# Performance work log

Hardware: AMD Instinct MI355X
Metric: run time of the kernel (lower is better)

Reference implementation:

```python
import jax, jax.numpy as jnp
import numpy as np

D_MODEL = 1024
D_STATE = 64
D_CONV = 4
EXPAND = 2
HEADDIM = 64
FFN_MULT = 3
MEM_DIM = 256
D_INNER = EXPAND * D_MODEL            # 2048
NHEADS = D_INNER // HEADDIM           # 32
CONV_DIM = D_INNER + 2 * D_STATE      # x, B, C channels through the causal conv
D_IN_PROJ = 2 * D_INNER + 2 * D_STATE + NHEADS  # z, xBC, dt
FFN_HID = FFN_MULT * D_MODEL


def _rms(x, eps=1e-6):
    return x * jax.lax.rsqrt(jnp.mean(x * x, axis=-1, keepdims=True) + eps)


def _mamba2(u, in_proj_w, conv_w, conv_b, dt_bias, A_log, D_param, mnorm_w, out_proj_w):
    # u: [B, L, d_model]
    Bsz, L, _ = u.shape
    zxbcdt = u @ in_proj_w.T                                  # [B, L, D_IN_PROJ]
    z = zxbcdt[..., :D_INNER]                                 # gate branch
    xBC = zxbcdt[..., D_INNER:D_INNER + CONV_DIM]
    dt = zxbcdt[..., D_INNER + CONV_DIM:]                     # [B, L, H]
    # causal depthwise conv1d (kernel D_CONV) + silu
    xp = jnp.pad(xBC, ((0, 0), (D_CONV - 1, 0), (0, 0)))
    xBC = sum(xp[:, k:k + L, :] * conv_w[:, k] for k in range(D_CONV)) + conv_b
    xBC = jax.nn.silu(xBC)
    xh = xBC[..., :D_INNER].reshape(Bsz, L, NHEADS, HEADDIM)  # [B, L, H, P]
    Bm = xBC[..., D_INNER:D_INNER + D_STATE]                  # [B, L, N] (ngroups=1)
    Cm = xBC[..., D_INNER + D_STATE:]                         # [B, L, N]
    dt = jax.nn.softplus(dt + dt_bias)                        # [B, L, H]
    dA = jnp.exp(dt * (-jnp.exp(A_log)))                      # [B, L, H]

    def step(h, inp):
        # h: [B, H, P, N]
        da, dtt, xt, bt, ct = inp
        h = da[:, :, None, None] * h + jnp.einsum('bh,bhp,bn->bhpn', dtt, xt, bt)
        y = jnp.einsum('bhpn,bn->bhp', h, ct)
        return h, y

    h0 = jnp.zeros((Bsz, NHEADS, HEADDIM, D_STATE), u.dtype)
    xs = (jnp.moveaxis(dA, 1, 0), jnp.moveaxis(dt, 1, 0), jnp.moveaxis(xh, 1, 0),
          jnp.moveaxis(Bm, 1, 0), jnp.moveaxis(Cm, 1, 0))
    _, ys = jax.lax.scan(step, h0, xs)                        # ys: [L, B, H, P]
    y = jnp.moveaxis(ys, 0, 1) + D_param[None, None, :, None] * xh
    y = y.reshape(Bsz, L, D_INNER)
    y = _rms(y * jax.nn.silu(z)) * mnorm_w                    # RMSNormGated
    return y @ out_proj_w.T


def setup_inputs() -> dict:
    key = jax.random.key(0)
    ks = jax.random.split(key, 12)
    B, L = 1, 2048
    s = 0.02
    return {
        'x': jax.random.normal(ks[0], (B, L, D_MODEL), jnp.float32),
        'x0': jax.random.normal(ks[1], (B, L, D_MODEL), jnp.float32),
        'mem': jax.random.normal(ks[2], (B, MEM_DIM), jnp.float32),
        'resid_mix': jnp.stack([jnp.ones(D_MODEL), jnp.zeros(D_MODEL)]),
        'ssm_scale': jnp.ones(D_MODEL),
        'mlp_scale': jnp.ones(D_MODEL),
        'ssm_norm_w': jnp.ones(D_MODEL),
        'ffn_norm_w': jnp.ones(D_MODEL),
        'in_proj_w': jax.random.normal(ks[3], (D_IN_PROJ, D_MODEL), jnp.float32) * s,
        'conv_w': jax.random.normal(ks[4], (CONV_DIM, D_CONV), jnp.float32) * 0.2,
        'conv_b': jnp.zeros(CONV_DIM),
        'dt_bias': jax.random.uniform(ks[5], (NHEADS,), jnp.float32, -2.0, 0.0),
        'A_log': jnp.log(jnp.linspace(1.0, 16.0, NHEADS).astype(jnp.float32)),
        'D_param': jnp.ones(NHEADS),
        'mnorm_w': jnp.ones(D_INNER),
        'out_proj_w': jax.random.normal(ks[6], (D_MODEL, D_INNER), jnp.float32) * s,
        'gate_up_w': jax.random.normal(ks[7], (2 * FFN_HID, D_MODEL), jnp.float32) * s,
        'down_w': jax.random.normal(ks[8], (D_MODEL, FFN_HID), jnp.float32) * s,
    }


def reference(x, x0, mem, resid_mix, ssm_scale, mlp_scale, ssm_norm_w, ffn_norm_w,
              in_proj_w, conv_w, conv_b, dt_bias, A_log, D_param, mnorm_w,
              out_proj_w, gate_up_w, down_w):
    # residual mixing (USE_MEMORY=0, so mem path is inert)
    x = resid_mix[0][None, None, :] * x + resid_mix[1][None, None, :] * x0
    y = _mamba2(_rms(x) * ssm_norm_w, in_proj_w, conv_w, conv_b, dt_bias,
                A_log, D_param, mnorm_w, out_proj_w)
    x = x + ssm_scale[None, None, :] * y
    # SwiGLU FFN
    h = _rms(x) * ffn_norm_w
    gu = h @ gate_up_w.T
    gate, up = jnp.split(gu, 2, axis=-1)
    x = x + mlp_scale[None, None, :] * ((jax.nn.silu(gate) * up) @ down_w.T)
    return x
```

## Files before the change

kernel.cpp:

```cpp
#include <hip/hip_runtime.h>
#include <hip/hip_bf16.h>
#include <math.h>

#define LSEQ 2048
#define DMODEL 1024
#define DINNER 2048
#define NHEADS 32
#define HEADDIM 64
#define DSTATE 64
#define CONVDIM 2176
#define XBCDT_W 2304
#define FFNHID 3072

typedef float f32x4 __attribute__((ext_vector_type(4)));
typedef __bf16 bf16x8 __attribute__((ext_vector_type(8)));
typedef __hip_bfloat16 bf16;

__device__ __forceinline__ float siluf(float x){ return x / (1.0f + expf(-x)); }

#define GLOAD_LDS16(gp, lp) __builtin_amdgcn_global_load_lds( \
    (const __attribute__((address_space(1))) void*)(gp), \
    (__attribute__((address_space(3))) void*)(lp), 16, 0, 0)

__device__ __forceinline__ float block_reduce_sum_256(float v){
  #pragma unroll
  for (int o = 32; o > 0; o >>= 1) v += __shfl_down(v, o, 64);
  __shared__ float sh[4];
  int lane = threadIdx.x & 63;
  int w = threadIdx.x >> 6;
  if (lane == 0) sh[w] = v;
  __syncthreads();
  return sh[0] + sh[1] + sh[2] + sh[3];
}

__device__ __forceinline__ ushort bf16bits(float f){
  __hip_bfloat16 h = __float2bfloat16(f);
  return *reinterpret_cast<ushort*>(&h);
}

__device__ __forceinline__ int swz64(int r, int c){
  return r*64 + ((((c>>3) ^ (r&7)))<<3) + (c&7);
}

__global__ __launch_bounds__(256) void k_castmix(
    const float* __restrict__ w0, const float* __restrict__ w1,
    const float* __restrict__ w2, const float* __restrict__ w3,
    bf16* __restrict__ d0, bf16* __restrict__ d1,
    bf16* __restrict__ d2, bf16* __restrict__ d3,
    const float* __restrict__ x, const float* __restrict__ x0,
    const float* __restrict__ rm, const float* __restrict__ nw,
    float* __restrict__ xres, bf16* __restrict__ u)
{
  int tid = threadIdx.x;
  if (blockIdx.x < 15616){
    int idx = blockIdx.x * 256 + tid;
    const float* s; bf16* d; int valid;
    if (idx < 1114112)      { s = w0; d = d0; valid = 1089536; }
    else if (idx < 1638400) { idx -= 1114112; s = w1; d = d1; valid = 524288; }
    else if (idx < 3211264) { idx -= 1638400; s = w2; d = d2; valid = 1572864; }
    else                    { idx -= 3211264; s = w3; d = d3; valid = 786432; }
    float4 v = (idx < valid) ? *(const float4*)(s + (size_t)idx * 4)
                             : make_float4(0.f, 0.f, 0.f, 0.f);
    ushort4 r;
    r.x = bf16bits(v.x); r.y = bf16bits(v.y); r.z = bf16bits(v.z); r.w = bf16bits(v.w);
    *(ushort4*)(d + (size_t)idx * 4) = r;
    return;
  }
  int row = blockIdx.x - 15616;
  float4 xv  = ((const float4*)(x  + (size_t)row * DMODEL))[tid];
  float4 x0v = ((const float4*)(x0 + (size_t)row * DMODEL))[tid];
  float4 r0 = ((const float4*)rm)[tid];
  float4 r1 = ((const float4*)(rm + DMODEL))[tid];
  float4 a;
  a.x = r0.x*xv.x + r1.x*x0v.x; a.y = r0.y*xv.y + r1.y*x0v.y;
  a.z = r0.z*xv.z + r1.z*x0v.z; a.w = r0.w*xv.w + r1.w*x0v.w;
  ((float4*)(xres + (size_t)row * DMODEL))[tid] = a;
  float ss = a.x*a.x + a.y*a.y + a.z*a.z + a.w*a.w;
  ss = block_reduce_sum_256(ss);
  float inv = rsqrtf(ss / (float)DMODEL + 1e-6f);
  float4 nv = ((const float4*)nw)[tid];
  ushort4 o;
  o.x = bf16bits(a.x*inv*nv.x); o.y = bf16bits(a.y*inv*nv.y);
  o.z = bf16bits(a.z*inv*nv.z); o.w = bf16bits(a.w*inv*nv.w);
  *(ushort4*)(u + (size_t)row * DMODEL + tid*4) = o;
}

__device__ __forceinline__ void xcdswz2(int &bx, int &by){
  int gx = gridDim.x;
  int nblk = gx * gridDim.y;
  int flat = by * gx + bx;
  flat = (flat & 7) * (nblk >> 3) + (flat >> 3);
  by = flat / gx; bx = flat - by * gx;
}

__device__ __forceinline__ void gemm_mainloop128(
    const bf16* __restrict__ A, const bf16* __restrict__ W,
    int ld, int Klen, bf16* As, bf16* Ws, f32x4 acc[4][4])
{
  int tid = threadIdx.x, lane = tid & 63, wid = tid >> 6;
  int wm = (wid >> 1) * 64, wn = (wid & 1) * 64;
  int r16 = lane & 15, g8 = lane >> 4;
  int srow = lane >> 2;
  int scol = ((lane & 3) ^ (srow & 3)) * 8;
  const bf16* ga0 = A + (size_t)(wid*32 + srow) * ld + scol;
  const bf16* ga1 = ga0 + (size_t)16 * ld;
  const bf16* gw0 = W + (size_t)(wid*32 + srow) * ld + scol;
  const bf16* gw1 = gw0 + (size_t)16 * ld;
  GLOAD_LDS16(ga0, As + wid*1024);
  GLOAD_LDS16(ga1, As + wid*1024 + 512);
  GLOAD_LDS16(gw0, Ws + wid*1024);
  GLOAD_LDS16(gw1, Ws + wid*1024 + 512);
  __syncthreads();
  int cur = 0, s4 = (r16 & 3) * 8;
  for (int k0 = 0; k0 < Klen; k0 += 32){
    if (k0 + 32 < Klen){
      int nb = (cur ^ 1) * 4096;
      GLOAD_LDS16(ga0 + k0 + 32, As + nb + wid*1024);
      GLOAD_LDS16(ga1 + k0 + 32, As + nb + wid*1024 + 512);
      GLOAD_LDS16(gw0 + k0 + 32, Ws + nb + wid*1024);
      GLOAD_LDS16(gw1 + k0 + 32, Ws + nb + wid*1024 + 512);
    }
    int cb = cur * 4096;
    bf16x8 af[4], bfr[4];
    #pragma unroll
    for (int i = 0; i < 4; ++i)
      af[i] = *(const bf16x8*)(As + cb + (wm + i*16 + r16)*32 + (g8*8 ^ s4));
    #pragma unroll
    for (int j = 0; j < 4; ++j)
      bfr[j] = *(const bf16x8*)(Ws + cb + (wn + j*16 + r16)*32 + (g8*8 ^ s4));
    #pragma unroll
    for (int i = 0; i < 4; ++i)
      #pragma unroll
      for (int j = 0; j < 4; ++j)
        acc[i][j] = __builtin_amdgcn_mfma_f32_16x16x32_bf16(af[i], bfr[j], acc[i][j], 0, 0, 0);
    __syncthreads();
    cur ^= 1;
  }
}

__global__ __launch_bounds__(256) void k_gemm_inproj(
    const bf16* __restrict__ A, const bf16* __restrict__ Wfull,
    float* __restrict__ zbuf, float* __restrict__ xbcdt)
{
  __shared__ __align__(16) bf16 As[2*4096];
  __shared__ __align__(16) bf16 Ws[2*4096];
  int bx = blockIdx.x, by = blockIdx.y;
  xcdswz2(bx, by);
  f32x4 acc[4][4];
  #pragma unroll
  for (int i = 0; i < 4; ++i)
    #pragma unroll
    for (int j = 0; j < 4; ++j) acc[i][j] = (f32x4){0.f,0.f,0.f,0.f};
  gemm_mainloop128(A + (size_t)(by*128)*DMODEL, Wfull + (size_t)(bx*128)*DMODEL,
                   DMODEL, DMODEL, As, Ws, acc);
  int tid = threadIdx.x, lane = tid & 63, wid = tid >> 6;
  int wm = (wid >> 1) * 64, wn = (wid & 1) * 64;
  int r16 = lane & 15, g8 = lane >> 4;
  float* Cp; int ldc, col0;
  if (bx < 16){ Cp = zbuf;  ldc = DINNER;  col0 = bx*128; }
  else        { Cp = xbcdt; ldc = XBCDT_W; col0 = (bx-16)*128; }
  #pragma unroll
  for (int i = 0; i < 4; ++i){
    int row = by*128 + wm + i*16 + g8*4;
    #pragma unroll
    for (int j = 0; j < 4; ++j){
      int col = col0 + wn + j*16 + r16;
      #pragma unroll
      for (int r = 0; r < 4; ++r)
        Cp[(size_t)(row + r) * ldc + col] = acc[i][j][r];
    }
  }
}

__global__ __launch_bounds__(256) void k_gemm_splitk(
    const bf16* __restrict__ A, const bf16* __restrict__ W,
    float* __restrict__ P, int Kfull, int Kq, int N)
{
  __shared__ __align__(16) bf16 As[2*4096];
  __shared__ __align__(16) bf16 Ws[2*4096];
  int gx = gridDim.x, gxy = gx * gridDim.y;
  int nblk = gxy * gridDim.z;
  int flat = blockIdx.z * gxy + blockIdx.y * gx + blockIdx.x;
  flat = (flat & 7) * (nblk >> 3) + (flat >> 3);
  int z = flat / gxy; int rem = flat - z * gxy;
  int by = rem / gx, bx = rem - by * gx;
  f32x4 acc[4][4];
  #pragma unroll
  for (int i = 0; i < 4; ++i)
    #pragma unroll
    for (int j = 0; j < 4; ++j) acc[i][j] = (f32x4){0.f,0.f,0.f,0.f};
  gemm_mainloop128(A + (size_t)(by*128)*Kfull + z*Kq,
                   W + (size_t)(bx*128)*Kfull + z*Kq,
                   Kfull, Kq, As, Ws, acc);
  float* Pz = P + (size_t)z * LSEQ * N;
  int tid = threadIdx.x, lane = tid & 63, wid = tid >> 6;
  int wm = (wid >> 1) * 64, wn = (wid & 1) * 64;
  int r16 = lane & 15, g8 = lane >> 4;
  #pragma unroll
  for (int i = 0; i < 4; ++i){
    int row = by*128 + wm + i*16 + g8*4;
    #pragma unroll
    for (int j = 0; j < 4; ++j){
      int col = bx*128 + wn + j*16 + r16;
      #pragma unroll
      for (int r = 0; r < 4; ++r)
        Pz[(size_t)(row + r) * N + col] = acc[i][j][r];
    }
  }
}

__global__ __launch_bounds__(256) void k_gemm_ffn(
    const bf16* __restrict__ A, const bf16* __restrict__ Wg, const bf16* __restrict__ Wu,
    bf16* __restrict__ act, int K)
{
  __shared__ __align__(16) bf16 As[2*4096];
  __shared__ __align__(16) bf16 Ws[2*4096];
  int bx = blockIdx.x, by = blockIdx.y;
  xcdswz2(bx, by);
  int tid = threadIdx.x, lane = tid & 63, wid = tid >> 6;
  int wm = (wid >> 1) * 64, wc = (wid & 1) * 32;
  int r16 = lane & 15, g8 = lane >> 4;
  int srow = lane >> 2;
  int scol = ((lane & 3) ^ (srow & 3)) * 8;
  const bf16* ga0 = A + (size_t)(by*128 + wid*32 + srow) * K + scol;
  const bf16* ga1 = ga0 + (size_t)16 * K;
  const bf16* gwsrc = (wid < 2) ? Wg : Wu;
  const bf16* gw0 = gwsrc + (size_t)(bx*64 + (wid & 1)*32 + srow) * K + scol;
  const bf16* gw1 = gw0 + (size_t)16 * K;
  f32x4 accg[4][2], accu[4][2];
  #pragma unroll
  for (int i = 0; i < 4; ++i)
    #pragma unroll
    for (int j = 0; j < 2; ++j){
      accg[i][j] = (f32x4){0.f,0.f,0.f,0.f};
      accu[i][j] = (f32x4){0.f,0.f,0.f,0.f};
    }
  GLOAD_LDS16(ga0, As + wid*1024);
  GLOAD_LDS16(ga1, As + wid*1024 + 512);
  GLOAD_LDS16(gw0, Ws + wid*1024);
  GLOAD_LDS16(gw1, Ws + wid*1024 + 512);
  __syncthreads();
  int cur = 0, s4 = (r16 & 3) * 8;
  for (int k0 = 0; k0 < K; k0 += 32){
    if (k0 + 32 < K){
      int nb = (cur ^ 1) * 4096;
      GLOAD_LDS16(ga0 + k0 + 32, As + nb + wid*1024);
      GLOAD_LDS16(ga1 + k0 + 32, As + nb + wid*1024 + 512);
      GLOAD_LDS16(gw0 + k0 + 32, Ws + nb + wid*1024);
      GLOAD_LDS16(gw1 + k0 + 32, Ws + nb + wid*1024 + 512);
    }
    int cb = cur * 4096;
    bf16x8 af[4], gf[2], uf[2];
    #pragma unroll
    for (int i = 0; i < 4; ++i)
      af[i] = *(const bf16x8*)(As + cb + (wm + i*16 + r16)*32 + (g8*8 ^ s4));
    #pragma unroll
    for (int j = 0; j < 2; ++j){
      int gr = wc + j*16 + r16;
      int ur = 64 + wc + j*16 + r16;
      gf[j] = *(const bf16x8*)(Ws + cb + gr*32 + (g8*8 ^ s4));
      uf[j] = *(const bf16x8*)(Ws + cb + ur*32 + (g8*8 ^ s4));
    }
    #pragma unroll
    for (int i = 0; i < 4; ++i)
      #pragma unroll
      for (int j = 0; j < 2; ++j){
        accg[i][j] = __builtin_amdgcn_mfma_f32_16x16x32_bf16(af[i], gf[j], accg[i][j], 0, 0, 0);
        accu[i][j] = __builtin_amdgcn_mfma_f32_16x16x32_bf16(af[i], uf[j], accu[i][j], 0, 0, 0);
      }
    __syncthreads();
    cur ^= 1;
  }
  #pragma unroll
  for (int i = 0; i < 4; ++i){
    int row = by*128 + wm + i*16 + g8*4;
    #pragma unroll
    for (int j = 0; j < 2; ++j){
      int col = bx*64 + wc + j*16 + r16;
      #pragma unroll
      for (int r = 0; r < 4; ++r){
        float g = accg[i][j][r], u = accu[i][j][r];
        act[(size_t)(row + r) * FFNHID + col] = __float2bfloat16(siluf(g) * u);
      }
    }
  }
}

__global__ __launch_bounds__(256) void k_convdt(
    const float* __restrict__ xbcdt, const float* __restrict__ cw,
    const float* __restrict__ cb, const float* __restrict__ dtb,
    const float* __restrict__ alog, float* __restrict__ xbc,
    float* __restrict__ dtv, float* __restrict__ lav)
{
  int idx = blockIdx.x * 256 + threadIdx.x;
  if (idx >= LSEQ * 2208) return;
  int l = idx / 2208, c = idx - l * 2208;
  if (c < CONVDIM){
    float acc = cb[c];
    #pragma unroll
    for (int k = 0; k < 4; ++k){
      int t = l + k - 3;
      if (t >= 0) acc = fmaf(xbcdt[(size_t)t * XBCDT_W + c], cw[c*4 + k], acc);
    }
    xbc[(size_t)l * CONVDIM + c] = siluf(acc);
  } else {
    int h = c - CONVDIM;
    float raw = xbcdt[(size_t)l * XBCDT_W + c] + dtb[h];
    float d = (raw > 20.f) ? raw : log1pf(expf(raw));
    dtv[l * NHEADS + h] = d;
    lav[l * NHEADS + h] = -expf(alog[h]) * d;
  }
}

__global__ __launch_bounds__(256) void k_scanA(
    const float* __restrict__ xbc, const float* __restrict__ dtv,
    const float* __restrict__ lav, float* __restrict__ T, float* __restrict__ ctot)
{
  __shared__ bf16 sXw[4096];
  __shared__ bf16 sBt[4096];
  __shared__ float scum[64], swt[64];
  int h = blockIdx.x >> 5, c = blockIdx.x & 31;
  int tid = threadIdx.x, t0 = c * 64;
  if (tid < 64){
    float cum = lav[(size_t)(t0 + tid) * NHEADS + h];
    #pragma unroll
    for (int o = 1; o < 64; o <<= 1){
      float v = __shfl_up(cum, o, 64);
      if (tid >= o) cum += v;
    }
    scum[tid] = cum;
  }
  __syncthreads();
  float Lc = scum[63];
  if (tid < 64)
    swt[tid] = expf(Lc - scum[tid]) * dtv[(size_t)(t0 + tid) * NHEADS + h];
  __syncthreads();
  for (int idx = tid; idx < 4096; idx += 256){
    int j = idx >> 6, n = idx & 63;
    size_t rb = (size_t)(t0 + j) * CONVDIM;
    sXw[swz64(n, j)] = __float2bfloat16(xbc[rb + h * HEADDIM + n] * swt[j]);
    sBt[swz64(n, j)] = __float2bfloat16(xbc[rb + DINNER + n]);
  }
  __syncthreads();
  int lane = tid & 63, wid = tid >> 6;
  int wr = (wid >> 1) * 32, wc = (wid & 1) * 32;
  int r16 = lane & 15, g8 = lane >> 4;
  f32x4 acc[2][2];
  #pragma unroll
  for (int i = 0; i < 2; ++i)
    #pragma unroll
    for (int j = 0; j < 2; ++j) acc[i][j] = (f32x4){0.f,0.f,0.f,0.f};
  #pragma unroll
  for (int kk = 0; kk < 2; ++kk){
    int ks = kk*4 + g8;
    bf16x8 a[2], b[2];
    #pragma unroll
    for (int i = 0; i < 2; ++i){
      int row = wr + i*16 + r16;
      a[i] = *(const bf16x8*)(sXw + row*64 + ((ks ^ (row&7))<<3));
    }
    #pragma unroll
    for (int j = 0; j < 2; ++j){
      int row = wc + j*16 + r16;
      b[j] = *(const bf16x8*)(sBt + row*64 + ((ks ^ (row&7))<<3));
    }
    #pragma unroll
    for (int i = 0; i < 2; ++i)
      #pragma unroll
      for (int j = 0; j < 2; ++j)
        acc[i][j] = __builtin_amdgcn_mfma_f32_16x16x32_bf16(a[i], b[j], acc[i][j], 0, 0, 0);
  }
  float* Tb = T + (size_t)blockIdx.x * 4096;
  #pragma unroll
  for (int i = 0; i < 2; ++i)
    #pragma unroll
    for (int j = 0; j < 2; ++j)
      #pragma unroll
      for (int r = 0; r < 4; ++r){
        int p = wr + i*16 + g8*4 + r, n = wc + j*16 + r16;
        Tb[p*64 + n] = acc[i][j][r];
      }
  if (tid == 0) ctot[blockIdx.x] = expf(Lc);
}

__global__ __launch_bounds__(256) void k_scanB(float* __restrict__ T, const float* __restrict__ ctot)
{
  int h = blockIdx.x >> 3, e = blockIdx.x & 7;
  int tid = threadIdx.x;
  size_t off = (size_t)e * 512 + tid * 2;
  float s0 = 0.f, s1 = 0.f;
  for (int c = 0; c < 32; ++c){
    float ct = ctot[h * 32 + c];
    size_t base = (size_t)(h * 32 + c) * 4096 + off;
    float2 tv = *(const float2*)&T[base];
    *(float2*)&T[base] = make_float2(s0, s1);
    s0 = fmaf(ct, s0, tv.x);
    s1 = fmaf(ct, s1, tv.y);
  }
}

__global__ __launch_bounds__(256) void k_scanC(
    const float* __restrict__ xbc, const float* __restrict__ Sin,
    const float* __restrict__ dtv, const float* __restrict__ lav,
    const float* __restrict__ Dp, float* __restrict__ y)
{
  __shared__ bf16 sC[4096];
  __shared__ bf16 sBS[4096];
  __shared__ bf16 sXt[4096];
  __shared__ bf16 sXr[4096];
  __shared__ bf16 sSb[4096];
  __shared__ float scum[64], sdt[64];
  int h = blockIdx.x >> 5, c = blockIdx.x & 31;
  int tid = threadIdx.x, t0 = c * 64;
  if (tid < 64){
    float cum = lav[(size_t)(t0 + tid) * NHEADS + h];
    #pragma unroll
    for (int o = 1; o < 64; o <<= 1){
      float v = __shfl_up(cum, o, 64);
      if (tid >= o) cum += v;
    }
    scum[tid] = cum;
    sdt[tid] = dtv[(size_t)(t0 + tid) * NHEADS + h];
  }
  for (int idx = tid; idx < 4096; idx += 256){
    int j = idx >> 6, n = idx & 63;
    size_t rb = (size_t)(t0 + j) * CONVDIM;
    float xv = xbc[rb + h * HEADDIM + n];
    sC [swz64(j, n)] = __float2bfloat16(xbc[rb + DINNER + DSTATE + n]);
    sBS[swz64(j, n)] = __float2bfloat16(xbc[rb + DINNER + n]);
    sXr[swz64(j, n)] = __float2bfloat16(xv);
    sXt[swz64(n, j)] = __float2bfloat16(xv);
    sSb[swz64(j, n)] = __float2bfloat16(Sin[(size_t)blockIdx.x * 4096 + idx]);
  }
  __syncthreads();
  int lane = tid & 63, wid = tid >> 6;
  int wr = (wid >> 1) * 32, wc = (wid & 1) * 32;
  int r16 = lane & 15, g8 = lane >> 4;
  f32x4 gacc[2][2];
  #pragma unroll
  for (int i = 0; i < 2; ++i)
    #pragma unroll
    for (int j = 0; j < 2; ++j) gacc[i][j] = (f32x4){0.f,0.f,0.f,0.f};
  #pragma unroll
  for (int kk = 0; kk < 2; ++kk){
    int ks = kk*4 + g8;
    bf16x8 a[2], b[2];
    #pragma unroll
    for (int i = 0; i < 2; ++i){
      int row = wr + i*16 + r16;
      a[i] = *(const bf16x8*)(sC + row*64 + ((ks ^ (row&7))<<3));
    }
    #pragma unroll
    for (int j = 0; j < 2; ++j){
      int row = wc + j*16 + r16;
      b[j] = *(const bf16x8*)(sBS + row*64 + ((ks ^ (row&7))<<3));
    }
    #pragma unroll
    for (int i = 0; i < 2; ++i)
      #pragma unroll
      for (int j = 0; j < 2; ++j)
        gacc[i][j] = __builtin_amdgcn_mfma_f32_16x16x32_bf16(a[i], b[j], gacc[i][j], 0, 0, 0);
  }
  __syncthreads();
  #pragma unroll
  for (int i = 0; i < 2; ++i)
    #pragma unroll
    for (int j = 0; j < 2; ++j)
      #pragma unroll
      for (int r = 0; r < 4; ++r){
        int i_ = wr + i*16 + g8*4 + r, j_ = wc + j*16 + r16;
        float v = (j_ <= i_) ? gacc[i][j][r] * expf(scum[i_] - scum[j_]) * sdt[j_] : 0.f;
        sBS[swz64(i_, j_)] = __float2bfloat16(v);
      }
  __syncthreads();
  f32x4 a1[2][2], a2[2][2];
  #pragma unroll
  for (int i = 0; i < 2; ++i)
    #pragma unroll
    for (int j = 0; j < 2; ++j){
      a1[i][j] = (f32x4){0.f,0.f,0.f,0.f};
      a2[i][j] = (f32x4){0.f,0.f,0.f,0.f};
    }
  #pragma unroll
  for (int kk = 0; kk < 2; ++kk){
    int ks = kk*4 + g8;
    bf16x8 sa[2], xa[2], ca[2], sb[2];
    #pragma unroll
    for (int i = 0; i < 2; ++i){
      int row = wr + i*16 + r16;
      sa[i] = *(const bf16x8*)(sBS + row*64 + ((ks ^ (row&7))<<3));
      ca[i] = *(const bf16x8*)(sC  + row*64 + ((ks ^ (row&7))<<3));
    }
    #pragma unroll
    for (int j = 0; j < 2; ++j){
      int row = wc + j*16 + r16;
      xa[j] = *(const bf16x8*)(sXt + row*64 + ((ks ^ (row&7))<<3));
      sb[j] = *(const bf16x8*)(sSb + row*64 + ((ks ^ (row&7))<<3));
    }
    #pragma unroll
    for (int i = 0; i < 2; ++i)
      #pragma unroll
      for (int j = 0; j < 2; ++j){
        a1[i][j] = __builtin_amdgcn_mfma_f32_16x16x32_bf16(sa[i], xa[j], a1[i][j], 0, 0, 0);
        a2[i][j] = __builtin_amdgcn_mfma_f32_16x16x32_bf16(ca[i], sb[j], a2[i][j], 0, 0, 0);
      }
  }
  float Dh = Dp[h];
  #pragma unroll
  for (int i = 0; i < 2; ++i)
    #pragma unroll
    for (int r = 0; r < 4; ++r){
      int i_ = wr + i*16 + g8*4 + r;
      float wi = expf(scum[i_]);
      #pragma unroll
      for (int j = 0; j < 2; ++j){
        int p_ = wc + j*16 + r16;
        float xv = __bfloat162float(sXr[swz64(i_, p_)]);
        y[(size_t)(t0 + i_) * DINNER + h * HEADDIM + p_] =
            a1[i][j][r] + wi * a2[i][j][r] + Dh * xv;
      }
    }
}

__global__ __launch_bounds__(256) void k_gate_rms(
    const float* __restrict__ y, const float* __restrict__ zbuf,
    const float* __restrict__ mw, bf16* __restrict__ yn)
{
  int row = blockIdx.x, tid = threadIdx.x;
  const float4* yr = (const float4*)(y    + (size_t)row * DINNER);
  const float4* zr = (const float4*)(zbuf + (size_t)row * DINNER);
  float4 v[2]; float ss = 0.f;
  #pragma unroll
  for (int i = 0; i < 2; ++i){
    int d4 = tid + i * 256;
    float4 yv = yr[d4], zv = zr[d4];
    float4 g;
    g.x = yv.x * siluf(zv.x); g.y = yv.y * siluf(zv.y);
    g.z = yv.z * siluf(zv.z); g.w = yv.w * siluf(zv.w);
    v[i] = g;
    ss += g.x*g.x + g.y*g.y + g.z*g.z + g.w*g.w;
  }
  ss = block_reduce_sum_256(ss);
  float inv = rsqrtf(ss / (float)DINNER + 1e-6f);
  #pragma unroll
  for (int i = 0; i < 2; ++i){
    int d4 = tid + i * 256;
    float4 mv = ((const float4*)mw)[d4];
    ushort4 o;
    o.x = bf16bits(v[i].x*inv*mv.x); o.y = bf16bits(v[i].y*inv*mv.y);
    o.z = bf16bits(v[i].z*inv*mv.z); o.w = bf16bits(v[i].w*inv*mv.w);
    *(ushort4*)(yn + (size_t)row * DINNER + d4*4) = o;
  }
}

__global__ __launch_bounds__(256) void k_res_rms(
    const float* __restrict__ xres, const float* __restrict__ yoP,
    const float* __restrict__ scale, const float* __restrict__ nw,
    float* __restrict__ x2, bf16* __restrict__ hb)
{
  int row = blockIdx.x, tid = threadIdx.x;
  const size_t PS = (size_t)LSEQ * DMODEL;
  float4 xv = ((const float4*)(xres + (size_t)row * DMODEL))[tid];
  float4 y0 = ((const float4*)(yoP          + (size_t)row * DMODEL))[tid];
  float4 y1 = ((const float4*)(yoP +   PS   + (size_t)row * DMODEL))[tid];
  float4 y2 = ((const float4*)(yoP + 2*PS   + (size_t)row * DMODEL))[tid];
  float4 y3 = ((const float4*)(yoP + 3*PS   + (size_t)row * DMODEL))[tid];
  float4 sv = ((const float4*)scale)[tid];
  float4 a;
  a.x = xv.x + sv.x*(y0.x+y1.x+y2.x+y3.x);
  a.y = xv.y + sv.y*(y0.y+y1.y+y2.y+y3.y);
  a.z = xv.z + sv.z*(y0.z+y1.z+y2.z+y3.z);
  a.w = xv.w + sv.w*(y0.w+y1.w+y2.w+y3.w);
  ((float4*)(x2 + (size_t)row * DMODEL))[tid] = a;
  float ss = a.x*a.x + a.y*a.y + a.z*a.z + a.w*a.w;
  ss = block_reduce_sum_256(ss);
  float inv = rsqrtf(ss / (float)DMODEL + 1e-6f);
  float4 nv = ((const float4*)nw)[tid];
  ushort4 o;
  o.x = bf16bits(a.x*inv*nv.x); o.y = bf16bits(a.y*inv*nv.y);
  o.z = bf16bits(a.z*inv*nv.z); o.w = bf16bits(a.w*inv*nv.w);
  *(ushort4*)(hb + (size_t)row * DMODEL + tid*4) = o;
}

__global__ __launch_bounds__(256) void k_final(
    const float* __restrict__ x2, const float* __restrict__ dP,
    const float* __restrict__ mscale, float* __restrict__ out)
{
  int i4 = blockIdx.x * 256 + threadIdx.x;
  const size_t PS4 = (size_t)LSEQ * DMODEL / 4;
  float4 xv = ((const float4*)x2)[i4];
  float4 a  = ((const float4*)dP)[i4];
  float4 b  = ((const float4*)dP)[i4 + PS4];
  float4 c  = ((const float4*)dP)[i4 + 2*PS4];
  float4 d  = ((const float4*)dP)[i4 + 3*PS4];
  float4 mv = ((const float4*)mscale)[i4 & 255];
  float4 o;
  o.x = xv.x + mv.x*(a.x+b.x+c.x+d.x);
  o.y = xv.y + mv.y*(a.y+b.y+c.y+d.y);
  o.z = xv.z + mv.z*(a.z+b.z+c.z+d.z);
  o.w = xv.w + mv.w*(a.w+b.w+c.w+d.w);
  ((float4*)out)[i4] = o;
}

extern "C" void kernel_launch(void* const* d_in, const int* in_sizes, int n_in,
                              void* d_out, int out_size, void* d_ws, size_t ws_size,
                              hipStream_t stream)
{
  const float* x      = (const float*)d_in[0];
  const float* x0     = (const float*)d_in[1];
  const float* rm     = (const float*)d_in[3];
  const float* sscale = (const float*)d_in[4];
  const float* mscale = (const float*)d_in[5];
  const float* snw    = (const float*)d_in[6];
  const float* fnw    = (const float*)d_in[7];
  const float* win    = (const float*)d_in[8];
  const float* cw     = (const float*)d_in[9];
  const float* cb     = (const float*)d_in[10];
  const float* dtb    = (const float*)d_in[11];
  const float* alog   = (const float*)d_in[12];
  const float* Dp     = (const float*)d_in[13];
  const float* mnw    = (const float*)d_in[14];
  const float* wout   = (const float*)d_in[15];
  const float* wgu    = (const float*)d_in[16];
  const float* wdn    = (const float*)d_in[17];
  float* out = (float*)d_out;

  const size_t MB = 1024ull * 1024ull;
  char* ws = (char*)d_ws;
  bf16*  woutb = (bf16*) (ws + 0*MB);
  bf16*  wgub  = (bf16*) (ws + 4*MB);
  bf16*  wdnb  = (bf16*) (ws + 16*MB);
  float* xres  = (float*)(ws + 22*MB);
  bf16*  winb  = (bf16*) (ws + 30*MB);
  bf16*  u     = (bf16*) (ws + 39*MB);
  float* dtv   = (float*)(ws + 39*MB);
  float* lav   = (float*)(ws + 39*MB + 256*1024);
  bf16*  hb    = (bf16*) (ws + 39*MB);
  float* zbuf  = (float*)(ws + 43*MB);
  float* x2    = (float*)(ws + 43*MB);
  float* xbcdt = (float*)(ws + 59*MB);
  float* yb    = (float*)(ws + 59*MB);
  float* yoP   = (float*)(ws + 59*MB);
  bf16*  act   = (bf16*) (ws + 59*MB);
  float* dP    = (float*)(ws + 71*MB);
  float* xbc   = (float*)(ws + 77*MB);
  float* T     = (float*)(ws + 95*MB);
  bf16*  yn    = (bf16*) (ws + 95*MB);
  float* ctot  = (float*)(ws + 112*MB);

  dim3 blk(256);
  k_castmix<<<17664, blk, 0, stream>>>(win, wout, wgu, wdn, winb, woutb, wgub, wdnb,
                                       x, x0, rm, snw, xres, u);
  k_gemm_inproj<<<dim3(34,16), blk, 0, stream>>>(u, winb, zbuf, xbcdt);
  k_convdt<<<(LSEQ*2208 + 255)/256, blk, 0, stream>>>(xbcdt, cw, cb, dtb, alog, xbc, dtv, lav);
  k_scanA<<<NHEADS*32, blk, 0, stream>>>(xbc, dtv, lav, T, ctot);
  k_scanB<<<NHEADS*8, blk, 0, stream>>>(T, ctot);
  k_scanC<<<NHEADS*32, blk, 0, stream>>>(xbc, T, dtv, lav, Dp, yb);
  k_gate_rms<<<LSEQ, blk, 0, stream>>>(yb, zbuf, mnw, yn);
  k_gemm_splitk<<<dim3(8,16,4), blk, 0, stream>>>(yn, woutb, yoP, DINNER, DINNER/4, DMODEL);
  k_res_rms<<<LSEQ, blk, 0, stream>>>(xres, yoP, sscale, fnw, x2, hb);
  k_gemm_ffn<<<dim3(48,16), blk, 0, stream>>>(hb, wgub, wgub + (size_t)FFNHID*DMODEL, act, DMODEL);
  k_gemm_splitk<<<dim3(8,16,4), blk, 0, stream>>>(act, wdnb, dP, FFNHID, FFNHID/4, DMODEL);
  k_final<<<2048, blk, 0, stream>>>(x2, dP, mscale, out);
}
```

Measured before the change: 211.7 us.

## Store SSM intermediates in bf16 and vectorize conv/scan loads

```diff
diff --git a/kernel.cpp b/kernel.cpp
--- a/kernel.cpp
+++ b/kernel.cpp
@@ -36,6 +36,9 @@
 __device__ __forceinline__ ushort bf16bits(float f){
   __hip_bfloat16 h = __float2bfloat16(f);
   return *reinterpret_cast<ushort*>(&h);
+}
+__device__ __forceinline__ float bfu(ushort u){
+  union { float f; unsigned int i; } w; w.i = ((unsigned int)u) << 16; return w.f;
 }
 
 __device__ __forceinline__ int swz64(int r, int c){
@@ -140,7 +143,7 @@
 
 __global__ __launch_bounds__(256) void k_gemm_inproj(
     const bf16* __restrict__ A, const bf16* __restrict__ Wfull,
-    float* __restrict__ zbuf, float* __restrict__ xbcdt)
+    bf16* __restrict__ zbuf, bf16* __restrict__ xbcdt)
 {
   __shared__ __align__(16) bf16 As[2*4096];
   __shared__ __align__(16) bf16 Ws[2*4096];
@@ -156,7 +159,7 @@
   int tid = threadIdx.x, lane = tid & 63, wid = tid >> 6;
   int wm = (wid >> 1) * 64, wn = (wid & 1) * 64;
   int r16 = lane & 15, g8 = lane >> 4;
-  float* Cp; int ldc, col0;
+  bf16* Cp; int ldc, col0;
   if (bx < 16){ Cp = zbuf;  ldc = DINNER;  col0 = bx*128; }
   else        { Cp = xbcdt; ldc = XBCDT_W; col0 = (bx-16)*128; }
   #pragma unroll
@@ -167,7 +170,7 @@
       int col = col0 + wn + j*16 + r16;
       #pragma unroll
       for (int r = 0; r < 4; ++r)
-        Cp[(size_t)(row + r) * ldc + col] = acc[i][j][r];
+        Cp[(size_t)(row + r) * ldc + col] = __float2bfloat16(acc[i][j][r]);
     }
   }
 }
@@ -287,37 +290,60 @@
 }
 
 __global__ __launch_bounds__(256) void k_convdt(
-    const float* __restrict__ xbcdt, const float* __restrict__ cw,
+    const bf16* __restrict__ xbcdt, const float* __restrict__ cw,
     const float* __restrict__ cb, const float* __restrict__ dtb,
-    const float* __restrict__ alog, float* __restrict__ xbc,
+    const float* __restrict__ alog, bf16* __restrict__ xbc,
     float* __restrict__ dtv, float* __restrict__ lav)
 {
   int idx = blockIdx.x * 256 + threadIdx.x;
-  if (idx >= LSEQ * 2208) return;
-  int l = idx / 2208, c = idx - l * 2208;
-  if (c < CONVDIM){
-    float acc = cb[c];
+  int l = idx / 552, q = idx - l * 552;
+  if (l >= LSEQ) return;
+  if (q < 544){
+    int c = q * 4;
+    float4 bv = *(const float4*)(cb + c);
+    float acc0 = bv.x, acc1 = bv.y, acc2 = bv.z, acc3 = bv.w;
+    float4 w0 = *(const float4*)(cw + (size_t)(c+0)*4);
+    float4 w1 = *(const float4*)(cw + (size_t)(c+1)*4);
+    float4 w2 = *(const float4*)(cw + (size_t)(c+2)*4);
+    float4 w3 = *(const float4*)(cw + (size_t)(c+3)*4);
+    const float* w0p = (const float*)&w0;
+    const float* w1p = (const float*)&w1;
+    const float* w2p = (const float*)&w2;
+    const float* w3p = (const float*)&w3;
     #pragma unroll
     for (int k = 0; k < 4; ++k){
       int t = l + k - 3;
-      if (t >= 0) acc = fmaf(xbcdt[(size_t)t * XBCDT_W + c], cw[c*4 + k], acc);
-    }
-    xbc[(size_t)l * CONVDIM + c] = siluf(acc);
+      if (t < 0) continue;
+      ushort4 rv = *(const ushort4*)(xbcdt + (size_t)t * XBCDT_W + c);
+      acc0 = fmaf(bfu(rv.x), w0p[k], acc0);
+      acc1 = fmaf(bfu(rv.y), w1p[k], acc1);
+      acc2 = fmaf(bfu(rv.z), w2p[k], acc2);
+      acc3 = fmaf(bfu(rv.w), w3p[k], acc3);
+    }
+    ushort4 o;
+    o.x = bf16bits(siluf(acc0)); o.y = bf16bits(siluf(acc1));
+    o.z = bf16bits(siluf(acc2)); o.w = bf16bits(siluf(acc3));
+    *(ushort4*)(xbc + (size_t)l * CONVDIM + c) = o;
   } else {
-    int h = c - CONVDIM;
-    float raw = xbcdt[(size_t)l * XBCDT_W + c] + dtb[h];
-    float d = (raw > 20.f) ? raw : log1pf(expf(raw));
-    dtv[l * NHEADS + h] = d;
-    lav[l * NHEADS + h] = -expf(alog[h]) * d;
+    int h0 = (q - 544) * 4;
+    ushort4 rv = *(const ushort4*)(xbcdt + (size_t)l * XBCDT_W + CONVDIM + h0);
+    float raws[4] = { bfu(rv.x), bfu(rv.y), bfu(rv.z), bfu(rv.w) };
+    #pragma unroll
+    for (int i = 0; i < 4; ++i){
+      float raw = raws[i] + dtb[h0 + i];
+      float d = (raw > 20.f) ? raw : log1pf(expf(raw));
+      dtv[l * NHEADS + h0 + i] = d;
+      lav[l * NHEADS + h0 + i] = -expf(alog[h0 + i]) * d;
+    }
   }
 }
 
 __global__ __launch_bounds__(256) void k_scanA(
-    const float* __restrict__ xbc, const float* __restrict__ dtv,
+    const bf16* __restrict__ xbc, const float* __restrict__ dtv,
     const float* __restrict__ lav, float* __restrict__ T, float* __restrict__ ctot)
 {
-  __shared__ bf16 sXw[4096];
-  __shared__ bf16 sBt[4096];
+  __shared__ __bf16 sXw[4096];
+  __shared__ __bf16 sBt[4096];
   __shared__ float scum[64], swt[64];
   int h = blockIdx.x >> 5, c = blockIdx.x & 31;
   int tid = threadIdx.x, t0 = c * 64;
@@ -335,11 +361,17 @@
   if (tid < 64)
     swt[tid] = expf(Lc - scum[tid]) * dtv[(size_t)(t0 + tid) * NHEADS + h];
   __syncthreads();
-  for (int idx = tid; idx < 4096; idx += 256){
-    int j = idx >> 6, n = idx & 63;
-    size_t rb = (size_t)(t0 + j) * CONVDIM;
-    sXw[swz64(n, j)] = __float2bfloat16(xbc[rb + h * HEADDIM + n] * swt[j]);
-    sBt[swz64(n, j)] = __float2bfloat16(xbc[rb + DINNER + n]);
+  for (int idx = tid; idx < 512; idx += 256){
+    int j = idx >> 3, n0 = (idx & 7) * 8;
+    const bf16* rb = xbc + (size_t)(t0 + j) * CONVDIM;
+    bf16x8 x8 = *(const bf16x8*)(rb + h * HEADDIM + n0);
+    bf16x8 b8 = *(const bf16x8*)(rb + DINNER + n0);
+    float wj = swt[j];
+    #pragma unroll
+    for (int e = 0; e < 8; ++e){
+      sXw[swz64(n0 + e, j)] = (__bf16)((float)x8[e] * wj);
+      sBt[swz64(n0 + e, j)] = b8[e];
+    }
   }
   __syncthreads();
   int lane = tid & 63, wid = tid >> 6;
@@ -400,15 +432,15 @@
 }
 
 __global__ __launch_bounds__(256) void k_scanC(
-    const float* __restrict__ xbc, const float* __restrict__ Sin,
+    const bf16* __restrict__ xbc, const float* __restrict__ Sin,
     const float* __restrict__ dtv, const float* __restrict__ lav,
-    const float* __restrict__ Dp, float* __restrict__ y)
-{
-  __shared__ bf16 sC[4096];
-  __shared__ bf16 sBS[4096];
-  __shared__ bf16 sXt[4096];
-  __shared__ bf16 sXr[4096];
-  __shared__ bf16 sSb[4096];
+    const float* __restrict__ Dp, bf16* __restrict__ y)
+{
+  __shared__ __bf16 sC[4096];
+  __shared__ __bf16 sBS[4096];
+  __shared__ __bf16 sXt[4096];
+  __shared__ __bf16 sXr[4096];
+  __shared__ __bf16 sSb[4096];
   __shared__ float scum[64], sdt[64];
   int h = blockIdx.x >> 5, c = blockIdx.x & 31;
   int tid = threadIdx.x, t0 = c * 64;
@@ -422,15 +454,25 @@
     scum[tid] = cum;
     sdt[tid] = dtv[(size_t)(t0 + tid) * NHEADS + h];
   }
-  for (int idx = tid; idx < 4096; idx += 256){
-    int j = idx >> 6, n = idx & 63;
-    size_t rb = (size_t)(t0 + j) * CONVDIM;
-    float xv = xbc[rb + h * HEADDIM + n];
-    sC [swz64(j, n)] = __float2bfloat16(xbc[rb + DINNER + DSTATE + n]);
-    sBS[swz64(j, n)] = __float2bfloat16(xbc[rb + DINNER + n]);
-    sXr[swz64(j, n)] = __float2bfloat16(xv);
-    sXt[swz64(n, j)] = __float2bfloat16(xv);
-    sSb[swz64(j, n)] = __float2bfloat16(Sin[(size_t)blockIdx.x * 4096 + idx]);
+  for (int idx = tid; idx < 512; idx += 256){
+    int j = idx >> 3, n0 = (idx & 7) * 8;
+    const bf16* rb = xbc + (size_t)(t0 + j) * CONVDIM;
+    bf16x8 x8 = *(const bf16x8*)(rb + h * HEADDIM + n0);
+    bf16x8 c8 = *(const bf16x8*)(rb + DINNER + DSTATE + n0);
+    bf16x8 b8 = *(const bf16x8*)(rb + DINNER + n0);
+    *(bf16x8*)(sC  + swz64(j, n0)) = c8;
+    *(bf16x8*)(sBS + swz64(j, n0)) = b8;
+    *(bf16x8*)(sXr + swz64(j, n0)) = x8;
+    const float* sp = Sin + (size_t)blockIdx.x * 4096 + j*64 + n0;
+    float4 s0 = *(const float4*)sp;
+    float4 s1 = *(const float4*)(sp + 4);
+    bf16x8 sv;
+    sv[0] = (__bf16)s0.x; sv[1] = (__bf16)s0.y; sv[2] = (__bf16)s0.z; sv[3] = (__bf16)s0.w;
+    sv[4] = (__bf16)s1.x; sv[5] = (__bf16)s1.y; sv[6] = (__bf16)s1.z; sv[7] = (__bf16)s1.w;
+    *(bf16x8*)(sSb + swz64(j, n0)) = sv;
+    #pragma unroll
+    for (int e = 0; e < 8; ++e)
+      sXt[swz64(n0 + e, j)] = x8[e];
   }
   __syncthreads();
   int lane = tid & 63, wid = tid >> 6;
@@ -470,7 +512,7 @@
       for (int r = 0; r < 4; ++r){
         int i_ = wr + i*16 + g8*4 + r, j_ = wc + j*16 + r16;
         float v = (j_ <= i_) ? gacc[i][j][r] * expf(scum[i_] - scum[j_]) * sdt[j_] : 0.f;
-        sBS[swz64(i_, j_)] = __float2bfloat16(v);
+        sBS[swz64(i_, j_)] = (__bf16)v;
       }
   __syncthreads();
   f32x4 a1[2][2], a2[2][2];
@@ -515,42 +557,38 @@
       #pragma unroll
       for (int j = 0; j < 2; ++j){
         int p_ = wc + j*16 + r16;
-        float xv = __bfloat162float(sXr[swz64(i_, p_)]);
+        float xv = (float)sXr[swz64(i_, p_)];
         y[(size_t)(t0 + i_) * DINNER + h * HEADDIM + p_] =
-            a1[i][j][r] + wi * a2[i][j][r] + Dh * xv;
+            __float2bfloat16(a1[i][j][r] + wi * a2[i][j][r] + Dh * xv);
       }
     }
 }
 
 __global__ __launch_bounds__(256) void k_gate_rms(
-    const float* __restrict__ y, const float* __restrict__ zbuf,
+    const bf16* __restrict__ y, const bf16* __restrict__ zbuf,
     const float* __restrict__ mw, bf16* __restrict__ yn)
 {
   int row = blockIdx.x, tid = threadIdx.x;
-  const float4* yr = (const float4*)(y    + (size_t)row * DINNER);
-  const float4* zr = (const float4*)(zbuf + (size_t)row * DINNER);
-  float4 v[2]; float ss = 0.f;
-  #pragma unroll
-  for (int i = 0; i < 2; ++i){
-    int d4 = tid + i * 256;
-    float4 yv = yr[d4], zv = zr[d4];
-    float4 g;
-    g.x = yv.x * siluf(zv.x); g.y = yv.y * siluf(zv.y);
-    g.z = yv.z * siluf(zv.z); g.w = yv.w * siluf(zv.w);
-    v[i] = g;
-    ss += g.x*g.x + g.y*g.y + g.z*g.z + g.w*g.w;
+  bf16x8 yv = *(const bf16x8*)(y    + (size_t)row * DINNER + tid*8);
+  bf16x8 zv = *(const bf16x8*)(zbuf + (size_t)row * DINNER + tid*8);
+  float g[8]; float ss = 0.f;
+  #pragma unroll
+  for (int e = 0; e < 8; ++e){
+    float gv = (float)yv[e] * siluf((float)zv[e]);
+    g[e] = gv; ss += gv * gv;
   }
   ss = block_reduce_sum_256(ss);
   float inv = rsqrtf(ss / (float)DINNER + 1e-6f);
-  #pragma unroll
-  for (int i = 0; i < 2; ++i){
-    int d4 = tid + i * 256;
-    float4 mv = ((const float4*)mw)[d4];
-    ushort4 o;
-    o.x = bf16bits(v[i].x*inv*mv.x); o.y = bf16bits(v[i].y*inv*mv.y);
-    o.z = bf16bits(v[i].z*inv*mv.z); o.w = bf16bits(v[i].w*inv*mv.w);
-    *(ushort4*)(yn + (size_t)row * DINNER + d4*4) = o;
-  }
+  float4 m0 = ((const float4*)mw)[tid*2];
+  float4 m1 = ((const float4*)mw)[tid*2 + 1];
+  const float* mp = (const float*)&m0;
+  bf16x8 o;
+  #pragma unroll
+  for (int e = 0; e < 4; ++e) o[e] = (__bf16)(g[e] * inv * mp[e]);
+  mp = (const float*)&m1;
+  #pragma unroll
+  for (int e = 0; e < 4; ++e) o[4+e] = (__bf16)(g[4+e] * inv * mp[e]);
+  *(bf16x8*)(yn + (size_t)row * DINNER + tid*8) = o;
 }
 
 __global__ __launch_bounds__(256) void k_res_rms(
@@ -636,14 +674,14 @@
   float* dtv   = (float*)(ws + 39*MB);
   float* lav   = (float*)(ws + 39*MB + 256*1024);
   bf16*  hb    = (bf16*) (ws + 39*MB);
-  float* zbuf  = (float*)(ws + 43*MB);
+  bf16*  zbuf  = (bf16*) (ws + 43*MB);
   float* x2    = (float*)(ws + 43*MB);
-  float* xbcdt = (float*)(ws + 59*MB);
-  float* yb    = (float*)(ws + 59*MB);
+  bf16*  xbcdt = (bf16*) (ws + 59*MB);
+  bf16*  yb    = (bf16*) (ws + 59*MB);
   float* yoP   = (float*)(ws + 59*MB);
   bf16*  act   = (bf16*) (ws + 59*MB);
   float* dP    = (float*)(ws + 71*MB);
-  float* xbc   = (float*)(ws + 77*MB);
+  bf16*  xbc   = (bf16*) (ws + 77*MB);
   float* T     = (float*)(ws + 95*MB);
   bf16*  yn    = (bf16*) (ws + 95*MB);
   float* ctot  = (float*)(ws + 112*MB);
@@ -652,7 +690,7 @@
   k_castmix<<<17664, blk, 0, stream>>>(win, wout, wgu, wdn, winb, woutb, wgub, wdnb,
                                        x, x0, rm, snw, xres, u);
   k_gemm_inproj<<<dim3(34,16), blk, 0, stream>>>(u, winb, zbuf, xbcdt);
-  k_convdt<<<(LSEQ*2208 + 255)/256, blk, 0, stream>>>(xbcdt, cw, cb, dtb, alog, xbc, dtv, lav);
+  k_convdt<<<(LSEQ*552)/256, blk, 0, stream>>>(xbcdt, cw, cb, dtb, alog, xbc, dtv, lav);
   k_scanA<<<NHEADS*32, blk, 0, stream>>>(xbc, dtv, lav, T, ctot);
   k_scanB<<<NHEADS*8, blk, 0, stream>>>(T, ctot);
   k_scanC<<<NHEADS*32, blk, 0, stream>>>(xbc, T, dtv, lav, Dp, yb);
```

Result: faster. 197.0 us (-6.9%).
